# Performance work log

Hardware: AMD Instinct MI355X
Metric: run time of the kernel (lower is better)

The kernel has to match this reference:

```python
import jax, jax.numpy as jnp
import numpy as np


def setup_inputs() -> dict:
    key = jax.random.key(0)
    kx, kw = jax.random.split(key)
    B, C, H = 32, 1024, 64
    x = jax.random.normal(kx, (B, C, H, H), dtype=jnp.float32)
    w = jax.random.normal(kw, (1, C), dtype=jnp.float32) * 0.02  # Linear(1024,1) weight
    b = jnp.zeros((1,), dtype=jnp.float32)                       # Linear bias
    mode = 0  # 0 == 'source' (label 0), 1 == 'target' (label 1)
    return {"x": x, "w": w, "b": b, "mode": mode}


def reference(x, w, b, mode):
    # fc1 applied at every spatial location: logits [B, H, W]
    logits = jnp.einsum('bchw,c->bhw', x, w[0]) + b[0]
    # Original applies Sigmoid, then BCEWithLogitsLoss (which sigmoids again).
    z = jax.nn.sigmoid(logits)
    y = jnp.asarray(mode, dtype=z.dtype)  # label: 0 for source, 1 for target
    # BCEWithLogits(z, y) = softplus(z) - z*y (stable since z in (0,1))
    per_elem = jax.nn.softplus(z) - z * y
    # sum over pixels of per-pixel batch mean, divided by H*W == global mean
    return jnp.mean(per_elem)
```

## Files before the change

kernel.cpp:

```cpp
#include <hip/hip_runtime.h>
#include <math.h>

constexpr int B_ = 32;
constexpr int C_ = 1024;
constexpr int HW = 64 * 64;
constexpr int NSPATIAL = B_ * HW;
constexpr int BLOCK = 256;
constexpr int PX_PER_BLOCK = 256;
constexpr int NBLOCKS = NSPATIAL / PX_PER_BLOCK;

__global__ __launch_bounds__(BLOCK) void k_main(
    const float4* __restrict__ x4, const float4* __restrict__ w4g,
    const float* __restrict__ bias, const int* __restrict__ mode,
    float* __restrict__ blocksum) {
    __shared__ float4 w4[C_ / 4];
    __shared__ float4 red[BLOCK];

    const int t    = threadIdx.x;
    const int wv   = t >> 6;
    const int lane = t & 63;

    w4[t] = w4g[t];
    __syncthreads();

    const int blk = blockIdx.x;
    const int b   = blk >> 4;
    const int hw4 = (blk & 15) * 64 + lane;

    const float4* p = x4 + ((size_t)(b * C_ + wv * 256) * (HW / 4)) + hw4;

    float4 acc = make_float4(0.f, 0.f, 0.f, 0.f);
    #pragma unroll 4
    for (int kk = 0; kk < 64; ++kk) {
        float4 wc = w4[wv * 64 + kk];
        float4 v0 = p[(size_t)(4 * kk + 0) * (HW / 4)];
        float4 v1 = p[(size_t)(4 * kk + 1) * (HW / 4)];
        float4 v2 = p[(size_t)(4 * kk + 2) * (HW / 4)];
        float4 v3 = p[(size_t)(4 * kk + 3) * (HW / 4)];
        acc.x += wc.x * v0.x + wc.y * v1.x + wc.z * v2.x + wc.w * v3.x;
        acc.y += wc.x * v0.y + wc.y * v1.y + wc.z * v2.y + wc.w * v3.y;
        acc.z += wc.x * v0.z + wc.y * v1.z + wc.z * v2.z + wc.w * v3.z;
        acc.w += wc.x * v0.w + wc.y * v1.w + wc.z * v2.w + wc.w * v3.w;
    }

    red[t] = acc;
    __syncthreads();

    if (t < 64) {
        float4 a0 = red[t], a1 = red[t + 64], a2 = red[t + 128], a3 = red[t + 192];
        const float bb = bias[0];
        const float y  = (float)mode[0];
        float logit[4] = {a0.x + a1.x + a2.x + a3.x,
                          a0.y + a1.y + a2.y + a3.y,
                          a0.z + a1.z + a2.z + a3.z,
                          a0.w + a1.w + a2.w + a3.w};
        float local = 0.f;
        #pragma unroll
        for (int j = 0; j < 4; ++j) {
            float lg = logit[j] + bb;
            float z  = 1.f / (1.f + __expf(-lg));
            local   += log1pf(__expf(z)) - z * y;
        }
        #pragma unroll
        for (int off = 32; off > 0; off >>= 1)
            local += __shfl_down(local, off, 64);
        if (lane == 0) blocksum[blk] = local;
    }
}

__global__ __launch_bounds__(512) void k_final(
    const float* __restrict__ blocksum, float* __restrict__ out) {
    __shared__ float red[512];
    const int t = threadIdx.x;
    red[t] = blocksum[t];
    __syncthreads();
    for (int off = 256; off > 0; off >>= 1) {
        if (t < off) red[t] += red[t + off];
        __syncthreads();
    }
    if (t == 0) out[0] = red[0] / (float)NSPATIAL;
}

extern "C" void kernel_launch(void* const* d_in, const int* in_sizes, int n_in,
                              void* d_out, int out_size, void* d_ws, size_t ws_size,
                              hipStream_t stream) {
    const float4* x4  = (const float4*)d_in[0];
    const float4* w4g = (const float4*)d_in[1];
    const float*  bia = (const float*)d_in[2];
    const int*    mod = (const int*)d_in[3];
    float* out = (float*)d_out;

    float* blocksum = (float*)d_ws;

    k_main<<<NBLOCKS, BLOCK, 0, stream>>>(x4, w4g, bia, mod, blocksum);
    k_final<<<1, 512, 0, stream>>>(blocksum, out);
}
```

Before: 97.35 us.

## Fuse final reduction via last-block atomic and use 8-wave blocks with nontemporal loads

Merges the second reduction kernel into the main kernel using an atomic ticket counter so the last finishing block performs the global sum. Block size doubles to 512 threads so each wave handles fewer channels, and input loads use nontemporal hints to avoid cache pollution. A memset is added each call to reset the counter, trading one kernel launch for a memset.

```diff
diff --git a/kernel.cpp b/kernel.cpp
--- a/kernel.cpp
+++ b/kernel.cpp
@@ -1,59 +1,62 @@
 #include <hip/hip_runtime.h>
 #include <math.h>
+
+typedef float v4f __attribute__((ext_vector_type(4)));
 
 constexpr int B_ = 32;
 constexpr int C_ = 1024;
 constexpr int HW = 64 * 64;
 constexpr int NSPATIAL = B_ * HW;
-constexpr int BLOCK = 256;
+constexpr int BLOCK = 512;
+constexpr int WAVES = 8;
+constexpr int CPW = C_ / WAVES;
 constexpr int PX_PER_BLOCK = 256;
 constexpr int NBLOCKS = NSPATIAL / PX_PER_BLOCK;
 
 __global__ __launch_bounds__(BLOCK) void k_main(
-    const float4* __restrict__ x4, const float4* __restrict__ w4g,
+    const v4f* __restrict__ x4, const v4f* __restrict__ w4g,
     const float* __restrict__ bias, const int* __restrict__ mode,
-    float* __restrict__ blocksum) {
-    __shared__ float4 w4[C_ / 4];
-    __shared__ float4 red[BLOCK];
+    float* __restrict__ blocksum, int* __restrict__ counter,
+    float* __restrict__ out) {
+    __shared__ v4f  w4[C_ / 4];
+    __shared__ v4f  red[BLOCK];
+    __shared__ float fred[NBLOCKS];
+    __shared__ int   s_last;
 
     const int t    = threadIdx.x;
     const int wv   = t >> 6;
     const int lane = t & 63;
 
-    w4[t] = w4g[t];
+    if (t < C_ / 4) w4[t] = w4g[t];
     __syncthreads();
 
     const int blk = blockIdx.x;
     const int b   = blk >> 4;
     const int hw4 = (blk & 15) * 64 + lane;
 
-    const float4* p = x4 + ((size_t)(b * C_ + wv * 256) * (HW / 4)) + hw4;
+    const v4f* p = x4 + ((size_t)(b * C_ + wv * CPW)) * (HW / 4) + hw4;
 
-    float4 acc = make_float4(0.f, 0.f, 0.f, 0.f);
+    v4f acc = (v4f)(0.f);
     #pragma unroll 4
-    for (int kk = 0; kk < 64; ++kk) {
-        float4 wc = w4[wv * 64 + kk];
-        float4 v0 = p[(size_t)(4 * kk + 0) * (HW / 4)];
-        float4 v1 = p[(size_t)(4 * kk + 1) * (HW / 4)];
-        float4 v2 = p[(size_t)(4 * kk + 2) * (HW / 4)];
-        float4 v3 = p[(size_t)(4 * kk + 3) * (HW / 4)];
-        acc.x += wc.x * v0.x + wc.y * v1.x + wc.z * v2.x + wc.w * v3.x;
-        acc.y += wc.x * v0.y + wc.y * v1.y + wc.z * v2.y + wc.w * v3.y;
-        acc.z += wc.x * v0.z + wc.y * v1.z + wc.z * v2.z + wc.w * v3.z;
-        acc.w += wc.x * v0.w + wc.y * v1.w + wc.z * v2.w + wc.w * v3.w;
+    for (int kk = 0; kk < CPW / 4; ++kk) {
+        v4f wc = w4[(wv * CPW) / 4 + kk];
+        v4f v0 = __builtin_nontemporal_load(&p[(size_t)(4 * kk + 0) * (HW / 4)]);
+        v4f v1 = __builtin_nontemporal_load(&p[(size_t)(4 * kk + 1) * (HW / 4)]);
+        v4f v2 = __builtin_nontemporal_load(&p[(size_t)(4 * kk + 2) * (HW / 4)]);
+        v4f v3 = __builtin_nontemporal_load(&p[(size_t)(4 * kk + 3) * (HW / 4)]);
+        acc += wc.x * v0 + wc.y * v1 + wc.z * v2 + wc.w * v3;
     }
 
     red[t] = acc;
     __syncthreads();
 
     if (t < 64) {
-        float4 a0 = red[t], a1 = red[t + 64], a2 = red[t + 128], a3 = red[t + 192];
+        v4f s = red[t];
+        #pragma unroll
+        for (int k = 1; k < WAVES; ++k) s += red[t + 64 * k];
         const float bb = bias[0];
         const float y  = (float)mode[0];
-        float logit[4] = {a0.x + a1.x + a2.x + a3.x,
-                          a0.y + a1.y + a2.y + a3.y,
-                          a0.z + a1.z + a2.z + a3.z,
-                          a0.w + a1.w + a2.w + a3.w};
+        float logit[4] = {s.x, s.y, s.z, s.w};
         float local = 0.f;
         #pragma unroll
         for (int j = 0; j < 4; ++j) {
@@ -66,32 +69,37 @@
             local += __shfl_down(local, off, 64);
         if (lane == 0) blocksum[blk] = local;
     }
-}
 
-__global__ __launch_bounds__(512) void k_final(
-    const float* __restrict__ blocksum, float* __restrict__ out) {
-    __shared__ float red[512];
-    const int t = threadIdx.x;
-    red[t] = blocksum[t];
+    if (t == 0) {
+        __threadfence();
+        int ticket = atomicAdd(counter, 1);
+        s_last = (ticket == NBLOCKS - 1) ? 1 : 0;
+    }
     __syncthreads();
-    for (int off = 256; off > 0; off >>= 1) {
-        if (t < off) red[t] += red[t + off];
+    if (s_last) {
+        __threadfence();
+        fred[t] = blocksum[t];
         __syncthreads();
+        for (int off = NBLOCKS / 2; off > 0; off >>= 1) {
+            if (t < off) fred[t] += fred[t + off];
+            __syncthreads();
+        }
+        if (t == 0) out[0] = fred[0] / (float)NSPATIAL;
     }
-    if (t == 0) out[0] = red[0] / (float)NSPATIAL;
 }
 
 extern "C" void kernel_launch(void* const* d_in, const int* in_sizes, int n_in,
                               void* d_out, int out_size, void* d_ws, size_t ws_size,
                               hipStream_t stream) {
-    const float4* x4  = (const float4*)d_in[0];
-    const float4* w4g = (const float4*)d_in[1];
-    const float*  bia = (const float*)d_in[2];
-    const int*    mod = (const int*)d_in[3];
+    const v4f*   x4  = (const v4f*)d_in[0];
+    const v4f*   w4g = (const v4f*)d_in[1];
+    const float* bia = (const float*)d_in[2];
+    const int*   mod = (const int*)d_in[3];
     float* out = (float*)d_out;
 
     float* blocksum = (float*)d_ws;
+    int*   counter  = (int*)((char*)d_ws + NBLOCKS * sizeof(float));
 
-    k_main<<<NBLOCKS, BLOCK, 0, stream>>>(x4, w4g, bia, mod, blocksum);
-    k_final<<<1, 512, 0, stream>>>(blocksum, out);
+    (void)hipMemsetAsync(counter, 0, sizeof(int), stream);
+    k_main<<<NBLOCKS, BLOCK, 0, stream>>>(x4, w4g, bia, mod, blocksum, counter, out);
 }
```

Result: slower. 113.0 us (+16.0%).
